# Optimization experiments

Hardware: AMD Instinct MI355X
Metric: run time of the kernel (lower is better)

## Reference

```python
import jax, jax.numpy as jnp
import numpy as np

B, T, C = 16, 2048, 384
E = 8          # num_experts
TOP_K = 2
CAP_F = 1.0
D_FF = 4 * C   # 1536


def setup_inputs() -> dict:
    key = jax.random.key(0)
    ks = jax.random.split(key, 10)
    s = 0.02
    return {
        "x": jax.random.normal(ks[0], (B, T, C), dtype=jnp.float32),
        "noise": jax.random.normal(ks[1], (B, T, E), dtype=jnp.float32),
        "w_route": jax.random.normal(ks[2], (C, E), dtype=jnp.float32) * s,
        "b_route": jnp.zeros((E,), dtype=jnp.float32),
        "w_noise": jax.random.normal(ks[3], (C, E), dtype=jnp.float32) * s,
        "b_noise": jnp.zeros((E,), dtype=jnp.float32),
        "w1": jax.random.normal(ks[4], (E, C, D_FF), dtype=jnp.float32) * s,
        "b1": jnp.zeros((E, D_FF), dtype=jnp.float32),
        "w2": jax.random.normal(ks[5], (E, D_FF, C), dtype=jnp.float32) * s,
        "b2": jnp.zeros((E, C), dtype=jnp.float32),
    }


def _moe_forward(x, noise, w_route, b_route, w_noise, b_noise, w1, b1, w2, b2):
    Bx, Tx, Cx = x.shape
    N = Bx * Tx
    cap = int(N * TOP_K / E * CAP_F)  # static expert capacity

    # --- NoisyTopkRouter ---
    logits = jnp.einsum('btc,ce->bte', x, w_route) + b_route
    noise_logits = jnp.einsum('btc,ce->bte', x, w_noise) + b_noise
    noisy = logits + noise * jax.nn.softplus(noise_logits)
    topv, topi = jax.lax.top_k(noisy, TOP_K)                    # [B,T,K]
    keep_mask = jnp.any(jax.nn.one_hot(topi, E, dtype=jnp.bool_), axis=-2)  # [B,T,E]
    sparse_logits = jnp.where(keep_mask, noisy, -jnp.inf)
    gating = jax.nn.softmax(sparse_logits, axis=-1)             # [B,T,E]

    # --- dispatch by top-1 expert with capacity drop (eval: dropout off) ---
    flat_x = x.reshape(N, Cx)
    flat_g = gating.reshape(N, E)
    top1 = jnp.argmax(flat_g, axis=-1)                          # [N]
    token_ids = jnp.arange(N, dtype=jnp.int32)
    out = jnp.zeros_like(flat_x)

    for i in range(E):
        mask = top1 == i                                        # [N]
        pos = jnp.cumsum(mask) - 1                              # rank within expert
        keep = mask & (pos < cap)
        slot = jnp.where(keep, pos, cap)                        # overflow -> dummy slot
        buf = jnp.zeros((cap + 1,), dtype=jnp.int32).at[slot].set(token_ids)
        idx = buf[:cap]                                         # token id per capacity slot
        valid = (jnp.arange(cap) < jnp.sum(keep))[:, None]      # [cap,1]
        xi = flat_x[idx]                                        # [cap,C] gather
        h = jnp.square(jax.nn.relu(xi @ w1[i] + b1[i]))         # ReLU^2
        yi = h @ w2[i] + b2[i]                                  # [cap,C]
        weighted = yi * flat_g[idx, i][:, None] * valid
        out = out.at[idx].add(weighted)                         # scatter-add

    return out.reshape(Bx, Tx, Cx)


def reference(x, noise, w_route, b_route, w_noise, b_noise, w1, b1, w2, b2):
    return _moe_forward(x, noise, w_route, b_route, w_noise, b_noise, w1, b1, w2, b2)
```

## Files before the change

kernel.cpp:

```cpp
#include <hip/hip_runtime.h>
#include <stdint.h>

#define E_NUM 8
#define CAP 8192
#define NTOK 32768
#define CDIM 384
#define DFF 1536
#define CNT_PAD 64

typedef unsigned short u16;
typedef __attribute__((ext_vector_type(8))) short short8;
typedef __attribute__((ext_vector_type(4))) float f32x4;

__device__ inline u16 f2bf(float f) {
    uint32_t u = __builtin_bit_cast(uint32_t, f);
    u += 0x7fffu + ((u >> 16) & 1u);
    return (u16)(u >> 16);
}

__device__ inline void gload_lds16(const void* g, void* l) {
    __builtin_amdgcn_global_load_lds(
        (const __attribute__((address_space(1))) void*)(uintptr_t)g,
        (__attribute__((address_space(3))) void*)(uint32_t)(uintptr_t)l,
        16, 0, 0);
}

__device__ inline float rsum_to_halves(float v) {
    int s;
    s = __builtin_bit_cast(int, v);
    v += __builtin_bit_cast(float, __builtin_amdgcn_update_dpp(0, s, 0x121, 0xF, 0xF, false));
    s = __builtin_bit_cast(int, v);
    v += __builtin_bit_cast(float, __builtin_amdgcn_update_dpp(0, s, 0x122, 0xF, 0xF, false));
    s = __builtin_bit_cast(int, v);
    v += __builtin_bit_cast(float, __builtin_amdgcn_update_dpp(0, s, 0x124, 0xF, 0xF, false));
    s = __builtin_bit_cast(int, v);
    v += __builtin_bit_cast(float, __builtin_amdgcn_update_dpp(0, s, 0x128, 0xF, 0xF, false));
    s = __builtin_bit_cast(int, v);
    v += __builtin_bit_cast(float, __builtin_amdgcn_ds_swizzle(s, 0x401F));
    return v;
}

__device__ inline float lane_total(float v) {
    int s = __builtin_bit_cast(int, v);
    return __builtin_bit_cast(float, __builtin_amdgcn_readlane(s, 0)) +
           __builtin_bit_cast(float, __builtin_amdgcn_readlane(s, 32));
}

__global__ __launch_bounds__(256, 1) void routing_kernel(
    const float* __restrict__ x, const float* __restrict__ noise,
    const float* __restrict__ w_route, const float* __restrict__ b_route,
    const float* __restrict__ w_noise, const float* __restrict__ b_noise,
    int* __restrict__ top1, float* __restrict__ gate)
{
    int lane = threadIdx.x & 63, w = threadIdx.x >> 6;
    float4 wr4[12], wn4[12];
#pragma unroll
    for (int i = 0; i < 6; ++i) {
        const float4* pr = (const float4*)(w_route + (size_t)(lane + 64 * i) * 8);
        const float4* pn = (const float4*)(w_noise + (size_t)(lane + 64 * i) * 8);
        wr4[2 * i] = pr[0]; wr4[2 * i + 1] = pr[1];
        wn4[2 * i] = pn[0]; wn4[2 * i + 1] = pn[1];
    }
    float br[E_NUM], bn[E_NUM];
#pragma unroll
    for (int e = 0; e < E_NUM; ++e) { br[e] = b_route[e]; bn[e] = b_noise[e]; }

    int tbase = blockIdx.x * 16 + w * 4;
#pragma unroll
    for (int tt = 0; tt < 4; ++tt) {
        int t = tbase + tt;
        const float* xr = x + (size_t)t * CDIM;
        float xv[6];
#pragma unroll
        for (int i = 0; i < 6; ++i) xv[i] = xr[lane + i * 64];
        float ar[E_NUM], an[E_NUM];
#pragma unroll
        for (int e = 0; e < E_NUM; ++e) { ar[e] = 0.f; an[e] = 0.f; }
#pragma unroll
        for (int i = 0; i < 6; ++i) {
            float4 r0 = wr4[2 * i], r1 = wr4[2 * i + 1];
            float4 n0 = wn4[2 * i], n1 = wn4[2 * i + 1];
            float xi = xv[i];
            ar[0] += xi * r0.x; ar[1] += xi * r0.y; ar[2] += xi * r0.z; ar[3] += xi * r0.w;
            ar[4] += xi * r1.x; ar[5] += xi * r1.y; ar[6] += xi * r1.z; ar[7] += xi * r1.w;
            an[0] += xi * n0.x; an[1] += xi * n0.y; an[2] += xi * n0.z; an[3] += xi * n0.w;
            an[4] += xi * n1.x; an[5] += xi * n1.y; an[6] += xi * n1.z; an[7] += xi * n1.w;
        }
        float nz[E_NUM];
        const float* np = noise + (size_t)t * E_NUM;
#pragma unroll
        for (int e = 0; e < E_NUM; ++e) {
            float sr = lane_total(rsum_to_halves(ar[e])) + br[e];
            float sn = lane_total(rsum_to_halves(an[e])) + bn[e];
            float sp = fmaxf(sn, 0.f) + __logf(1.f + __expf(-fabsf(sn)));
            nz[e] = sr + np[e] * sp;
        }
        float v1 = -1e30f; int i1 = 0;
#pragma unroll
        for (int e = 0; e < E_NUM; ++e) if (nz[e] > v1) { v1 = nz[e]; i1 = e; }
        float v2 = -1e30f;
#pragma unroll
        for (int e = 0; e < E_NUM; ++e) if (e != i1 && nz[e] > v2) v2 = nz[e];
        if (lane == 0) {
            gate[t] = 1.f / (1.f + __expf(v2 - v1));
            top1[t] = i1;
        }
    }
}

__global__ __launch_bounds__(256) void build_lists_kernel(
    const int* __restrict__ top1, int* __restrict__ cnt, int* __restrict__ list)
{
    int t = blockIdx.x * 256 + threadIdx.x;
    int lane = threadIdx.x & 63;
    int e1 = top1[t];
#pragma unroll
    for (int e = 0; e < E_NUM; ++e) {
        unsigned long long m = __ballot(e1 == e);
        if (m == 0) continue;
        int c = __popcll(m);
        int leader = __ffsll((long long)m) - 1;
        int base = 0;
        if (lane == leader) base = atomicAdd(&cnt[e * CNT_PAD], c);
        base = __shfl(base, leader);
        if (e1 == e) {
            int pos = base + __popcll(m & ((1ull << lane) - 1ull));
            if (pos < CAP) list[e * CAP + pos] = t;
        }
    }
}

__global__ void offsets_kernel(const int* __restrict__ cnt, int* __restrict__ offs)
{
    if (threadIdx.x == 0 && blockIdx.x == 0) {
        int o = 0;
        for (int e = 0; e < E_NUM; ++e) {
            offs[e] = o;
            int n = min(cnt[e * CNT_PAD], CAP);
            o += (n + 127) & ~127;
        }
    }
}

__global__ __launch_bounds__(256) void transpose_cvt_kernel(
    const float* __restrict__ in, u16* __restrict__ out, int R, int S)
{
    __shared__ float tile[32][33];
    size_t eoff = (size_t)blockIdx.z * R * S;
    const float* ip = in + eoff;
    u16* op = out + eoff;
    int c0 = blockIdx.x * 32, r0 = blockIdx.y * 32;
    int tx = threadIdx.x, ty = threadIdx.y;
#pragma unroll
    for (int i = ty; i < 32; i += 8)
        tile[i][tx] = ip[(size_t)(r0 + i) * S + (c0 + tx)];
    __syncthreads();
#pragma unroll
    for (int i = ty; i < 32; i += 8)
        op[(size_t)(c0 + i) * R + (r0 + tx)] = f2bf(tile[tx][i]);
}

__global__ __launch_bounds__(256) void gather_kernel(
    const float* __restrict__ x, const int* __restrict__ list,
    const int* __restrict__ cnt, const int* __restrict__ offs,
    u16* __restrict__ Xg)
{
    int e = blockIdx.z;
    const int* le = list + (size_t)e * CAP;
    int n = min(cnt[e * CNT_PAD], CAP);
    int w = threadIdx.x >> 6, lane = threadIdx.x & 63;
    int row = blockIdx.x * 4 + w;
    int pad = (n + 127) & ~127;
    if (row >= pad) return;
    u16* orow = Xg + (size_t)(offs[e] + row) * CDIM;
    if (row < n) {
        const float* xr = x + (size_t)le[row] * CDIM;
#pragma unroll
        for (int i = 0; i < CDIM / 64; ++i) orow[lane + i * 64] = f2bf(xr[lane + i * 64]);
    } else {
#pragma unroll
        for (int i = 0; i < CDIM / 64; ++i) orow[lane + i * 64] = 0;
    }
}

template <int KD, int ND, bool FFN1>
__global__ __launch_bounds__(256, 4) void gemm_kernel(
    const u16* __restrict__ A, const u16* __restrict__ Bt,
    const float* __restrict__ bias, u16* __restrict__ H, float* __restrict__ Out,
    const int* __restrict__ cnt, const int* __restrict__ offs,
    const int* __restrict__ list, const float* __restrict__ gate)
{
    constexpr int NT = ND / 128;
    int bid = blockIdx.x;
    int xcd = bid & 7, slot = bid >> 3;
    int n_idx = slot % NT;
    int mglob = xcd + 8 * (slot / NT);
    int e = mglob >> 6;
    int m0 = (mglob & 63) * 128;
    int n_e = min(cnt[e * CNT_PAD], CAP);
    int pad_e = (n_e + 127) & ~127;
    if (m0 >= pad_e) return;
    int base = offs[e];
    const u16* Ae = A + (size_t)(base + m0) * KD;
    const u16* Be = Bt + ((size_t)e * ND + (size_t)n_idx * 128) * KD;

    __shared__ __align__(16) u16 As[128 * 64];
    __shared__ __align__(16) u16 Bs[128 * 64];

    int tid = threadIdx.x;
    int w = tid >> 6, lane = tid & 63;
    int quad = lane >> 4, l15 = lane & 15;
    int wr = w & 1, wc = w >> 1;

    int srow = tid >> 3;
    int gcol = ((tid & 7) ^ ((tid >> 3) & 7)) * 8;

    f32x4 acc[4][4];
    f32x4 zero = {0.f, 0.f, 0.f, 0.f};
#pragma unroll
    for (int a = 0; a < 4; ++a)
#pragma unroll
        for (int b = 0; b < 4; ++b) acc[a][b] = zero;

    for (int kb = 0; kb < KD / 64; ++kb) {
#pragma unroll
        for (int i = 0; i < 4; ++i) {
            int row = i * 32 + srow;
            gload_lds16(Ae + (size_t)row * KD + kb * 64 + gcol, &As[i * 2048 + tid * 8]);
            gload_lds16(Be + (size_t)row * KD + kb * 64 + gcol, &Bs[i * 2048 + tid * 8]);
        }
        __syncthreads();
#pragma unroll
        for (int h = 0; h < 2; ++h) {
            int pga = (((h * 4 + quad) ^ (l15 & 7))) * 8;
            short8 af[4], bf[4];
#pragma unroll
            for (int t = 0; t < 4; ++t) {
                af[t] = *(const short8*)&As[(wr * 64 + t * 16 + l15) * 64 + pga];
                bf[t] = *(const short8*)&Bs[(wc * 64 + t * 16 + l15) * 64 + pga];
            }
#pragma unroll
            for (int mt = 0; mt < 4; ++mt)
#pragma unroll
                for (int nt = 0; nt < 4; ++nt)
                    acc[mt][nt] = __builtin_amdgcn_mfma_f32_16x16x32_bf16(
                        af[mt], bf[nt], acc[mt][nt], 0, 0, 0);
        }
        __syncthreads();
    }

    int n0 = n_idx * 128;
    if (FFN1) {
        u16* He = H + (size_t)(base + m0) * ND;
#pragma unroll
        for (int mt = 0; mt < 4; ++mt) {
            int rowL = wr * 64 + mt * 16 + quad * 4;
#pragma unroll
            for (int nt = 0; nt < 4; ++nt) {
                int col = n0 + wc * 64 + nt * 16 + l15;
                float b = bias[(size_t)e * ND + col];
#pragma unroll
                for (int r = 0; r < 4; ++r) {
                    float v = acc[mt][nt][r] + b;
                    v = fmaxf(v, 0.f);
                    v = v * v;
                    He[(size_t)(rowL + r) * ND + col] = f2bf(v);
                }
            }
        }
    } else {
#pragma unroll
        for (int mt = 0; mt < 4; ++mt) {
            int rowL = wr * 64 + mt * 16 + quad * 4;
#pragma unroll
            for (int r = 0; r < 4; ++r) {
                int rr = m0 + rowL + r;
                if (rr < n_e) {
                    int tok = list[(size_t)e * CAP + rr];
                    float g = gate[tok];
#pragma unroll
                    for (int nt = 0; nt < 4; ++nt) {
                        int col = n0 + wc * 64 + nt * 16 + l15;
                        float v = acc[mt][nt][r] + bias[(size_t)e * ND + col];
                        Out[(size_t)tok * CDIM + col] = v * g;
                    }
                }
            }
        }
    }
}

extern "C" void kernel_launch(void* const* d_in, const int* in_sizes, int n_in,
                              void* d_out, int out_size, void* d_ws, size_t ws_size,
                              hipStream_t stream)
{
    const float* x       = (const float*)d_in[0];
    const float* noise   = (const float*)d_in[1];
    const float* w_route = (const float*)d_in[2];
    const float* b_route = (const float*)d_in[3];
    const float* w_noise = (const float*)d_in[4];
    const float* b_noise = (const float*)d_in[5];
    const float* w1      = (const float*)d_in[6];
    const float* b1      = (const float*)d_in[7];
    const float* w2      = (const float*)d_in[8];
    const float* b2      = (const float*)d_in[9];
    float* out = (float*)d_out;

    char* ws = (char*)d_ws;
    size_t off = 0;
    auto alloc = [&](size_t bytes) {
        char* p = ws + off;
        off += (bytes + 255) & ~(size_t)255;
        return p;
    };
    int*   cnt  = (int*)alloc((size_t)E_NUM * CNT_PAD * sizeof(int));
    int*   top1 = (int*)alloc((size_t)NTOK * sizeof(int));
    int*   list = (int*)alloc((size_t)E_NUM * CAP * sizeof(int));
    float* gate = (float*)alloc((size_t)NTOK * sizeof(float));
    int*   offs = (int*)alloc((size_t)(E_NUM + 1) * sizeof(int));
    u16*   W1t  = (u16*)alloc((size_t)E_NUM * DFF * CDIM * 2);
    u16*   W2t  = (u16*)alloc((size_t)E_NUM * CDIM * DFF * 2);

    size_t rows = NTOK + E_NUM * 128;
    u16* Xg = (u16*)alloc(rows * CDIM * 2);
    u16* Hb = (u16*)alloc(rows * DFF * 2);

    hipMemsetAsync(cnt, 0, (size_t)E_NUM * CNT_PAD * sizeof(int), stream);
    hipMemsetAsync(d_out, 0, (size_t)out_size * sizeof(float), stream);

    routing_kernel<<<NTOK / 16, 256, 0, stream>>>(x, noise, w_route, b_route,
                                                  w_noise, b_noise, top1, gate);
    build_lists_kernel<<<NTOK / 256, 256, 0, stream>>>(top1, cnt, list);
    transpose_cvt_kernel<<<dim3(DFF / 32, CDIM / 32, E_NUM), dim3(32, 8), 0, stream>>>(
        w1, W1t, CDIM, DFF);
    transpose_cvt_kernel<<<dim3(CDIM / 32, DFF / 32, E_NUM), dim3(32, 8), 0, stream>>>(
        w2, W2t, DFF, CDIM);
    offsets_kernel<<<1, 64, 0, stream>>>(cnt, offs);
    gather_kernel<<<dim3(CAP / 4, 1, E_NUM), 256, 0, stream>>>(x, list, cnt, offs, Xg);

    gemm_kernel<CDIM, DFF, true><<<dim3((DFF / 128) * 512), 256, 0, stream>>>(
        Xg, W1t, b1, Hb, nullptr, cnt, offs, nullptr, nullptr);
    gemm_kernel<DFF, CDIM, false><<<dim3((CDIM / 128) * 512), 256, 0, stream>>>(
        Hb, W2t, b2, nullptr, out, cnt, offs, list, gate);
}
```

Measured before the change: 313.6 us.

## Double-buffer GEMM tiles via register prefetch and zero only dropped output rows

Replaces the direct global-to-LDS loads in the expert GEMM with a register-staged, double-buffered LDS pipeline. The next K tiles are loaded into registers while the current tile is computed, which removes one barrier per iteration. LDS use doubles and occupancy is lowered to 2 blocks per CU. It also drops the full memset of the output: only tokens that overflow expert capacity get their rows zeroed in build_lists, relying on the FFN2 epilogue writing every kept token's row directly.

```diff
diff --git a/kernel.cpp b/kernel.cpp
--- a/kernel.cpp
+++ b/kernel.cpp
@@ -16,13 +16,6 @@
     uint32_t u = __builtin_bit_cast(uint32_t, f);
     u += 0x7fffu + ((u >> 16) & 1u);
     return (u16)(u >> 16);
-}
-
-__device__ inline void gload_lds16(const void* g, void* l) {
-    __builtin_amdgcn_global_load_lds(
-        (const __attribute__((address_space(1))) void*)(uintptr_t)g,
-        (__attribute__((address_space(3))) void*)(uint32_t)(uintptr_t)l,
-        16, 0, 0);
 }
 
 __device__ inline float rsum_to_halves(float v) {
@@ -109,7 +102,8 @@
 }
 
 __global__ __launch_bounds__(256) void build_lists_kernel(
-    const int* __restrict__ top1, int* __restrict__ cnt, int* __restrict__ list)
+    const int* __restrict__ top1, int* __restrict__ cnt, int* __restrict__ list,
+    float* __restrict__ out)
 {
     int t = blockIdx.x * 256 + threadIdx.x;
     int lane = threadIdx.x & 63;
@@ -125,7 +119,12 @@
         base = __shfl(base, leader);
         if (e1 == e) {
             int pos = base + __popcll(m & ((1ull << lane) - 1ull));
-            if (pos < CAP) list[e * CAP + pos] = t;
+            if (pos < CAP) {
+                list[e * CAP + pos] = t;
+            } else {
+                float* orow = out + (size_t)t * CDIM;
+                for (int i = 0; i < CDIM; ++i) orow[i] = 0.f;
+            }
         }
     }
 }
@@ -184,13 +183,14 @@
 }
 
 template <int KD, int ND, bool FFN1>
-__global__ __launch_bounds__(256, 4) void gemm_kernel(
+__global__ __launch_bounds__(256, 2) void gemm_kernel(
     const u16* __restrict__ A, const u16* __restrict__ Bt,
     const float* __restrict__ bias, u16* __restrict__ H, float* __restrict__ Out,
     const int* __restrict__ cnt, const int* __restrict__ offs,
     const int* __restrict__ list, const float* __restrict__ gate)
 {
     constexpr int NT = ND / 128;
+    constexpr int NI = KD / 64;
     int bid = blockIdx.x;
     int xcd = bid & 7, slot = bid >> 3;
     int n_idx = slot % NT;
@@ -204,8 +204,8 @@
     const u16* Ae = A + (size_t)(base + m0) * KD;
     const u16* Be = Bt + ((size_t)e * ND + (size_t)n_idx * 128) * KD;
 
-    __shared__ __align__(16) u16 As[128 * 64];
-    __shared__ __align__(16) u16 Bs[128 * 64];
+    __shared__ __align__(16) u16 As[2][128 * 64];
+    __shared__ __align__(16) u16 Bs[2][128 * 64];
 
     int tid = threadIdx.x;
     int w = tid >> 6, lane = tid & 63;
@@ -222,22 +222,32 @@
 #pragma unroll
         for (int b = 0; b < 4; ++b) acc[a][b] = zero;
 
-    for (int kb = 0; kb < KD / 64; ++kb) {
+    float4 rA[2][4], rB[2][4];
+
+    auto loadT = [&](int kb, int P) {
 #pragma unroll
         for (int i = 0; i < 4; ++i) {
             int row = i * 32 + srow;
-            gload_lds16(Ae + (size_t)row * KD + kb * 64 + gcol, &As[i * 2048 + tid * 8]);
-            gload_lds16(Be + (size_t)row * KD + kb * 64 + gcol, &Bs[i * 2048 + tid * 8]);
-        }
-        __syncthreads();
+            rA[P][i] = *(const float4*)(Ae + (size_t)row * KD + kb * 64 + gcol);
+            rB[P][i] = *(const float4*)(Be + (size_t)row * KD + kb * 64 + gcol);
+        }
+    };
+    auto wlds = [&](int P) {
+#pragma unroll
+        for (int i = 0; i < 4; ++i) {
+            *(float4*)&As[P][i * 2048 + tid * 8] = rA[P][i];
+            *(float4*)&Bs[P][i * 2048 + tid * 8] = rB[P][i];
+        }
+    };
+    auto compute = [&](int P) {
 #pragma unroll
         for (int h = 0; h < 2; ++h) {
             int pga = (((h * 4 + quad) ^ (l15 & 7))) * 8;
             short8 af[4], bf[4];
 #pragma unroll
             for (int t = 0; t < 4; ++t) {
-                af[t] = *(const short8*)&As[(wr * 64 + t * 16 + l15) * 64 + pga];
-                bf[t] = *(const short8*)&Bs[(wc * 64 + t * 16 + l15) * 64 + pga];
+                af[t] = *(const short8*)&As[P][(wr * 64 + t * 16 + l15) * 64 + pga];
+                bf[t] = *(const short8*)&Bs[P][(wc * 64 + t * 16 + l15) * 64 + pga];
             }
 #pragma unroll
             for (int mt = 0; mt < 4; ++mt)
@@ -246,7 +256,25 @@
                     acc[mt][nt] = __builtin_amdgcn_mfma_f32_16x16x32_bf16(
                         af[mt], bf[nt], acc[mt][nt], 0, 0, 0);
         }
+    };
+
+    loadT(0, 0);
+    loadT(1, 1);
+    wlds(0);
+    __syncthreads();
+
+#pragma unroll 1
+    for (int kb = 0; kb < NI; kb += 2) {
+        if (kb + 2 < NI) loadT(kb + 2, 0);
+        compute(0);
+        wlds(1);
         __syncthreads();
+        if (kb + 3 < NI) loadT(kb + 3, 1);
+        compute(1);
+        if (kb + 2 < NI) {
+            wlds(0);
+            __syncthreads();
+        }
     }
 
     int n0 = n_idx * 128;
@@ -326,11 +354,10 @@
     u16* Hb = (u16*)alloc(rows * DFF * 2);
 
     hipMemsetAsync(cnt, 0, (size_t)E_NUM * CNT_PAD * sizeof(int), stream);
-    hipMemsetAsync(d_out, 0, (size_t)out_size * sizeof(float), stream);
 
     routing_kernel<<<NTOK / 16, 256, 0, stream>>>(x, noise, w_route, b_route,
                                                   w_noise, b_noise, top1, gate);
-    build_lists_kernel<<<NTOK / 256, 256, 0, stream>>>(top1, cnt, list);
+    build_lists_kernel<<<NTOK / 256, 256, 0, stream>>>(top1, cnt, list, out);
     transpose_cvt_kernel<<<dim3(DFF / 32, CDIM / 32, E_NUM), dim3(32, 8), 0, stream>>>(
         w1, W1t, CDIM, DFF);
     transpose_cvt_kernel<<<dim3(CDIM / 32, DFF / 32, E_NUM), dim3(32, 8), 0, stream>>>(
```

Result: slower. 648.7 us (+106.9%).
